# Performance work log

Measured on AMD Instinct MI355X. Metric: run time of the kernel, lower is better.

The kernel has to match this reference:

```python
import jax, jax.numpy as jnp
import numpy as np

N, T, H = 4000, 32, 64      # N = batch_size*n_neurons, t_repetition, gcn_d
E = 1024000
NT = N * T                   # graph nodes after temporal unrolling
N_NEURONS = 500
B = N // N_NEURONS
T_EBD = 16                   # tau * t_repetition = 0.5*32
N_STEPS = 12


def setup_inputs() -> dict:
    key = jax.random.key(0)
    ks = jax.random.split(key, 13)
    s = 1.0 / np.sqrt(H)
    return {
        "node_features": jax.random.normal(ks[0], (N, T, H), jnp.float32),
        "edge_index_batch": jax.random.randint(ks[1], (2, E), 0, NT, jnp.int32),
        "edge_attr_batch": jax.random.uniform(ks[2], (E,), jnp.float32),
        "batch": jax.random.randint(ks[3], (N,), 0, B, jnp.int32),
        # GRU params (1 layer, torch layout: W_ih [3H,H], W_hh [3H,H])
        "gru_Wih": jax.random.normal(ks[4], (3 * H, H), jnp.float32) * s,
        "gru_Whh": jax.random.normal(ks[5], (3 * H, H), jnp.float32) * s,
        "gru_bih": jax.random.normal(ks[6], (3 * H,), jnp.float32) * s,
        "gru_bhh": jax.random.normal(ks[7], (3 * H,), jnp.float32) * s,
        # GCNConv linear weight [out,in], no bias
        "gcn_W": jax.random.normal(ks[8], (H, H), jnp.float32) * s,
        # temporal attention MLP: Linear(T->T_ebd), Linear(T_ebd->T), no bias
        "attn_W1": jax.random.normal(ks[9], (T_EBD, T), jnp.float32) * (1.0 / np.sqrt(T)),
        "attn_W2": jax.random.normal(ks[10], (T, T_EBD), jnp.float32) * (1.0 / np.sqrt(T_EBD)),
        # final head Linear(gcn_d -> n_steps) with bias
        "fc_W": jax.random.normal(ks[11], (N_STEPS, H), jnp.float32) * s,
        "fc_b": jax.random.normal(ks[12], (N_STEPS,), jnp.float32) * s,
    }


def _gru(x, Wih, Whh, bih, bhh):
    # x: [N, T, H] -> outputs [N, T, H] (torch GRU equations, h0 = 0)
    xg = x @ Wih.T + bih  # [N, T, 3H], input projection precomputed

    def step(h, xg_t):
        hg = h @ Whh.T + bhh
        xr, xz, xn = jnp.split(xg_t, 3, axis=-1)
        hr, hz, hn = jnp.split(hg, 3, axis=-1)
        r = jax.nn.sigmoid(xr + hr)
        z = jax.nn.sigmoid(xz + hz)
        n = jnp.tanh(xn + r * hn)
        h_new = (1.0 - z) * n + z * h
        return h_new, h_new

    h0 = jnp.zeros((x.shape[0], Whh.shape[1]), x.dtype)
    _, hs = jax.lax.scan(step, h0, jnp.swapaxes(xg, 0, 1))  # hs: [T, N, H]
    return jnp.swapaxes(hs, 0, 1)


def _gcn(x, W, edge_index, edge_weight, n_nodes):
    # PyG GCNConv: add self-loops (weight 1), symmetric deg^-1/2 norm, no bias
    loops = jnp.arange(n_nodes, dtype=edge_index.dtype)
    src = jnp.concatenate([edge_index[0], loops])
    dst = jnp.concatenate([edge_index[1], loops])
    w = jnp.concatenate([edge_weight, jnp.ones((n_nodes,), edge_weight.dtype)])
    xw = x @ W.T                                            # [NT, H]
    deg = jax.ops.segment_sum(w, dst, num_segments=n_nodes)
    dis = jnp.where(deg > 0, jax.lax.rsqrt(jnp.where(deg > 0, deg, 1.0)), 0.0)
    norm = dis[src] * w * dis[dst]                          # [E+NT]
    msgs = norm[:, None] * xw[src]                          # gather + scale
    return jax.ops.segment_sum(msgs, dst, num_segments=n_nodes)


def reference(node_features, edge_index_batch, edge_attr_batch, batch,
              gru_Wih, gru_Whh, gru_bih, gru_bhh, gcn_W,
              attn_W1, attn_W2, fc_W, fc_b):
    # DGRLayer: GRU over time, then GCN over the flattened (node,time) graph
    g = _gru(node_features, gru_Wih, gru_Whh, gru_bih, gru_bhh)  # [N, T, H]
    x = g.reshape(NT, H)
    x = _gcn(x, gcn_W, edge_index_batch, edge_attr_batch, NT)
    x3 = x.reshape(N, T, H)

    # TemporalAttention (reshape mirrors torch contiguous .view semantics)
    xt = x3.reshape(B, T, N_NEURONS * H).mean(axis=-1)           # [B, T]
    attn = jax.nn.sigmoid(jax.nn.relu(xt @ attn_W1.T) @ attn_W2.T)  # [B, T]

    nf = x3.reshape(B, T, N_NEURONS, H)
    pooled = jnp.sum(attn[:, :, None, None] * nf, axis=(1, 2))   # [B, H]
    return pooled @ fc_W.T + fc_b                                # [B, n_steps]
```

## Files before the change

### kernel.cpp

```cpp
#include <hip/hip_runtime.h>
#include <hip/hip_fp16.h>

#define NNODES   4000
#define TSTEPS   32
#define HDIM     64
#define ECOUNT   1024000
#define NTOT     128000
#define BATCHB   8
#define NNEUR    500
#define TEBD     16
#define NSTEPS   12

#define CNT_SHIFT 44
#define SUM_MASK  ((1ull << CNT_SHIFT) - 1ull)
#define SLOTS     32
#define REC_BLOCKS (NNODES / 16)

typedef _Float16 half8_t __attribute__((ext_vector_type(8)));
typedef float    f32x4_t __attribute__((ext_vector_type(4)));

__device__ __forceinline__ float sigmoidf_(float x) {
    return 1.0f / (1.0f + __expf(-x));
}
__device__ __forceinline__ float tanhf_(float x) {
    return 1.0f - 2.0f / (1.0f + __expf(2.0f * x));
}

__global__ __launch_bounds__(256) void k_recHist(
    const float* __restrict__ x, const float* __restrict__ Wih,
    const float* __restrict__ Whh, const float* __restrict__ bih,
    const float* __restrict__ bhh, const float* __restrict__ Wg,
    _Float16* __restrict__ xwh,
    const int* __restrict__ ei, const float* __restrict__ ea,
    unsigned long long* __restrict__ dc, int2* __restrict__ se32)
{
    __shared__ __align__(16) _Float16 hbuf[2][16 * 72];

    const int tid = threadIdx.x;

    if (blockIdx.x >= REC_BLOCKS) {
        int e = (blockIdx.x - REC_BLOCKS) * 256 + tid;
        int s = ei[e], d = ei[ECOUNT + e];
        float w = ea[e];
        unsigned long long fx = (unsigned long long)(w * 4294967296.0f + 0.5f);
        unsigned long long old = atomicAdd(&dc[d], (1ull << CNT_SHIFT) | fx);
        int r = (int)(old >> CNT_SHIFT);
        if (r < SLOTS)
            se32[d * SLOTS + r] = make_int2(s, __float_as_int(w));
        return;
    }

    const int lane = tid & 63;
    const int wv   = tid >> 6;
    const int c    = lane & 15;
    const int quad = lane >> 4;
    const int n0   = blockIdx.x * 16;

    auto makeB = [&](const float* W, int row, int k0) -> half8_t {
        const float4* p = (const float4*)(W + (size_t)row * HDIM + k0);
        float4 u = p[0], v = p[1];
        half8_t h;
        h[0] = (_Float16)u.x; h[1] = (_Float16)u.y; h[2] = (_Float16)u.z; h[3] = (_Float16)u.w;
        h[4] = (_Float16)v.x; h[5] = (_Float16)v.y; h[6] = (_Float16)v.z; h[7] = (_Float16)v.w;
        return h;
    };

    half8_t Bxr[2], Bxz[2], Bxn[2], Bhr[2], Bhz[2], Bhn[2], Bw[2];
#pragma unroll
    for (int kt = 0; kt < 2; ++kt) {
        int k0 = kt * 32 + quad * 8;
        Bxr[kt] = makeB(Wih, wv * 16 + c, k0);
        Bxz[kt] = makeB(Wih, 64 + wv * 16 + c, k0);
        Bxn[kt] = makeB(Wih, 128 + wv * 16 + c, k0);
        Bhr[kt] = makeB(Whh, wv * 16 + c, k0);
        Bhz[kt] = makeB(Whh, 64 + wv * 16 + c, k0);
        Bhn[kt] = makeB(Whh, 128 + wv * 16 + c, k0);
        Bw[kt]  = makeB(Wg, wv * 16 + c, k0);
    }

    const int f = wv * 16 + c;
    const float brz_r = bih[f] + bhh[f];
    const float brz_z = bih[64 + f] + bhh[64 + f];
    const float bin_  = bih[128 + f];
    const float bhn_  = bhh[128 + f];

    float hreg[4] = {0.f, 0.f, 0.f, 0.f};
    half8_t ah[2];

    const float* xp = x + (size_t)(n0 + c) * (TSTEPS * HDIM) + quad * 8;

    float4 xq0[4], xq1[4];
    {
        const float* p0 = xp;
        xq0[0] = *(const float4*)(p0);      xq0[1] = *(const float4*)(p0 + 4);
        xq0[2] = *(const float4*)(p0 + 32); xq0[3] = *(const float4*)(p0 + 36);
        const float* p1 = xp + HDIM;
        xq1[0] = *(const float4*)(p1);      xq1[1] = *(const float4*)(p1 + 4);
        xq1[2] = *(const float4*)(p1 + 32); xq1[3] = *(const float4*)(p1 + 36);
    }

    auto step = [&](int t, float4* xq) {
        half8_t ax[2];
#pragma unroll
        for (int kt = 0; kt < 2; ++kt) {
            float4 u = xq[kt * 2], v = xq[kt * 2 + 1];
            half8_t a;
            a[0] = (_Float16)u.x; a[1] = (_Float16)u.y; a[2] = (_Float16)u.z; a[3] = (_Float16)u.w;
            a[4] = (_Float16)v.x; a[5] = (_Float16)v.y; a[6] = (_Float16)v.z; a[7] = (_Float16)v.w;
            ax[kt] = a;
        }
        if (t + 2 < TSTEPS) {
            const float* pt = xp + (size_t)(t + 2) * HDIM;
            xq[0] = *(const float4*)(pt);      xq[1] = *(const float4*)(pt + 4);
            xq[2] = *(const float4*)(pt + 32); xq[3] = *(const float4*)(pt + 36);
        }

        f32x4_t Cr  = (f32x4_t){0.f, 0.f, 0.f, 0.f};
        f32x4_t Cz  = (f32x4_t){0.f, 0.f, 0.f, 0.f};
        f32x4_t Cnx = (f32x4_t){0.f, 0.f, 0.f, 0.f};
        f32x4_t Cnh = (f32x4_t){0.f, 0.f, 0.f, 0.f};

#pragma unroll
        for (int kt = 0; kt < 2; ++kt) {
            Cr  = __builtin_amdgcn_mfma_f32_16x16x32_f16(ax[kt], Bxr[kt], Cr, 0, 0, 0);
            Cz  = __builtin_amdgcn_mfma_f32_16x16x32_f16(ax[kt], Bxz[kt], Cz, 0, 0, 0);
            Cnx = __builtin_amdgcn_mfma_f32_16x16x32_f16(ax[kt], Bxn[kt], Cnx, 0, 0, 0);
        }
        if (t > 0) {
#pragma unroll
            for (int kt = 0; kt < 2; ++kt) {
                Cr  = __builtin_amdgcn_mfma_f32_16x16x32_f16(ah[kt], Bhr[kt], Cr, 0, 0, 0);
                Cz  = __builtin_amdgcn_mfma_f32_16x16x32_f16(ah[kt], Bhz[kt], Cz, 0, 0, 0);
                Cnh = __builtin_amdgcn_mfma_f32_16x16x32_f16(ah[kt], Bhn[kt], Cnh, 0, 0, 0);
            }
        }

        _Float16* hb = hbuf[t & 1];
#pragma unroll
        for (int r = 0; r < 4; ++r) {
            float rr = sigmoidf_(Cr[r] + brz_r);
            float zz = sigmoidf_(Cz[r] + brz_z);
            float nn = tanhf_(Cnx[r] + bin_ + rr * (Cnh[r] + bhn_));
            float hn = (1.0f - zz) * nn + zz * hreg[r];
            hreg[r] = hn;
            hb[(quad * 4 + r) * 72 + f] = (_Float16)hn;
        }

        __syncthreads();

#pragma unroll
        for (int kt = 0; kt < 2; ++kt)
            ah[kt] = *(half8_t*)&hb[c * 72 + kt * 32 + quad * 8];

        f32x4_t Cw = (f32x4_t){0.f, 0.f, 0.f, 0.f};
#pragma unroll
        for (int kt = 0; kt < 2; ++kt)
            Cw = __builtin_amdgcn_mfma_f32_16x16x32_f16(ah[kt], Bw[kt], Cw, 0, 0, 0);

#pragma unroll
        for (int r = 0; r < 4; ++r) {
            int row = (n0 + quad * 4 + r) * TSTEPS + t;
            xwh[(size_t)row * HDIM + f] = (_Float16)Cw[r];
        }
    };

#pragma unroll 1
    for (int tt = 0; tt < TSTEPS; tt += 2) {
        step(tt, xq0);
        step(tt + 1, xq1);
    }
}

__global__ void k_dis(const unsigned long long* __restrict__ dc,
                      float* __restrict__ dis) {
    int i = blockIdx.x * blockDim.x + threadIdx.x;
    if (i < NTOT) {
        float deg = 1.0f + (float)(dc[i] & SUM_MASK) * 0x1p-32f;
        dis[i] = rsqrtf(deg);
    }
}

__global__ __launch_bounds__(256) void k_gather(
    const _Float16* __restrict__ xwh, const unsigned long long* __restrict__ dc,
    const int2* __restrict__ se32, const float* __restrict__ dis,
    _Float16* __restrict__ y)
{
    const int lane = threadIdx.x & 63;
    const int d = blockIdx.x * 4 + (threadIdx.x >> 6);
    const float dd = dis[d];
    int cnt = (int)(dc[d] >> CNT_SHIFT);
    cnt = cnt < SLOTS ? cnt : SLOTS;
    const int2* bkt = se32 + (size_t)d * SLOTS;

    float a0 = dd * (float)xwh[(size_t)d * HDIM + lane];
    float a1 = 0.f, a2 = 0.f, a3 = 0.f;
    int j = 0;
    for (; j + 4 <= cnt; j += 4) {
        int2 e0 = bkt[j], e1 = bkt[j + 1], e2 = bkt[j + 2], e3 = bkt[j + 3];
        float c0 = dis[e0.x] * __int_as_float(e0.y);
        float c1 = dis[e1.x] * __int_as_float(e1.y);
        float c2 = dis[e2.x] * __int_as_float(e2.y);
        float c3 = dis[e3.x] * __int_as_float(e3.y);
        float v0 = (float)xwh[(size_t)e0.x * HDIM + lane];
        float v1 = (float)xwh[(size_t)e1.x * HDIM + lane];
        float v2 = (float)xwh[(size_t)e2.x * HDIM + lane];
        float v3 = (float)xwh[(size_t)e3.x * HDIM + lane];
        a0 = fmaf(c0, v0, a0);
        a1 = fmaf(c1, v1, a1);
        a2 = fmaf(c2, v2, a2);
        a3 = fmaf(c3, v3, a3);
    }
    for (; j < cnt; ++j) {
        int2 e = bkt[j];
        a0 = fmaf(dis[e.x] * __int_as_float(e.y),
                  (float)xwh[(size_t)e.x * HDIM + lane], a0);
    }
    y[(size_t)d * HDIM + lane] = (_Float16)(dd * ((a0 + a1) + (a2 + a3)));
}

__global__ __launch_bounds__(256) void k_S(const _Float16* __restrict__ y,
                                           float* __restrict__ S) {
    const int bt = blockIdx.x;
    const int tid = threadIdx.x;
    const int h = tid & 63, g = tid >> 6;
    const _Float16* base = y + (size_t)bt * (NNEUR * HDIM);
    float acc = 0.f;
    for (int n = g; n < NNEUR; n += 4) acc += (float)base[n * HDIM + h];
    __shared__ float red[256];
    red[tid] = acc;
    __syncthreads();
    if (tid < 64)
        S[bt * 64 + tid] = red[tid] + red[64 + tid] + red[128 + tid] + red[192 + tid];
}

__global__ __launch_bounds__(256) void k_final(
    const float* __restrict__ S, const float* __restrict__ W1,
    const float* __restrict__ W2, const float* __restrict__ fcW,
    const float* __restrict__ fcb, float* __restrict__ out)
{
    __shared__ float xt[256];
    __shared__ float a1[128];
    __shared__ float attn[256];
    __shared__ float pooled[512];
    const int tid = threadIdx.x;

    {
        float s = 0.f;
        const float* p = S + tid * 64;
#pragma unroll
        for (int hh = 0; hh < 64; ++hh) s += p[hh];
        xt[tid] = s * (1.0f / 32000.0f);
    }
    __syncthreads();
    if (tid < 128) {
        int b = tid >> 4, i = tid & 15;
        float s = 0.f;
#pragma unroll
        for (int t = 0; t < 32; ++t) s += xt[b * 32 + t] * W1[i * 32 + t];
        a1[tid] = fmaxf(s, 0.f);
    }
    __syncthreads();
    {
        int b = tid >> 5, t = tid & 31;
        float s = 0.f;
#pragma unroll
        for (int i = 0; i < 16; ++i) s += a1[b * 16 + i] * W2[t * 16 + i];
        attn[tid] = 1.0f / (1.0f + __expf(-s));
    }
    __syncthreads();
    for (int o = tid; o < 512; o += 256) {
        int b = o >> 6, h = o & 63;
        float s = 0.f;
#pragma unroll
        for (int t = 0; t < 32; ++t) s += attn[b * 32 + t] * S[(b * 32 + t) * 64 + h];
        pooled[o] = s;
    }
    __syncthreads();
    if (tid < BATCHB * NSTEPS) {
        int b = tid / NSTEPS, st = tid % NSTEPS;
        float acc = fcb[st];
#pragma unroll
        for (int h = 0; h < 64; ++h) acc += pooled[b * 64 + h] * fcW[st * 64 + h];
        out[b * NSTEPS + st] = acc;
    }
}

extern "C" void kernel_launch(void* const* d_in, const int* in_sizes, int n_in,
                              void* d_out, int out_size, void* d_ws, size_t ws_size,
                              hipStream_t stream) {
    const float* x   = (const float*)d_in[0];
    const int*   ei  = (const int*)  d_in[1];
    const float* ea  = (const float*)d_in[2];
    const float* Wih = (const float*)d_in[4];
    const float* Whh = (const float*)d_in[5];
    const float* bih = (const float*)d_in[6];
    const float* bhh = (const float*)d_in[7];
    const float* Wg  = (const float*)d_in[8];
    const float* W1  = (const float*)d_in[9];
    const float* W2  = (const float*)d_in[10];
    const float* fcW = (const float*)d_in[11];
    const float* fcb = (const float*)d_in[12];
    float* out = (float*)d_out;

    char* p = (char*)d_ws;
    unsigned long long* dc = (unsigned long long*)p; p += sizeof(unsigned long long) * NTOT;
    int2*  se32 = (int2*)p;        p += sizeof(int2) * (size_t)NTOT * SLOTS;
    _Float16* xwh = (_Float16*)p;  p += sizeof(_Float16) * (size_t)NTOT * HDIM;
    _Float16* y   = (_Float16*)p;  p += sizeof(_Float16) * (size_t)NTOT * HDIM;
    float* dis = (float*)p;        p += sizeof(float) * NTOT;
    float* S   = (float*)p;

    hipMemsetAsync(dc, 0, sizeof(unsigned long long) * NTOT, stream);
    k_recHist <<<REC_BLOCKS + ECOUNT / 256, 256, 0, stream>>>(
        x, Wih, Whh, bih, bhh, Wg, xwh, ei, ea, dc, se32);
    k_dis     <<<(NTOT + 255) / 256, 256, 0, stream>>>(dc, dis);
    k_gather  <<<NTOT / 4, 256, 0, stream>>>(xwh, dc, se32, dis, y);
    k_S       <<<256, 256, 0, stream>>>(y, S);
    k_final   <<<1, 256, 0, stream>>>(S, W1, W2, fcW, fcb, out);
}
```

Baseline: 273.3 us.

## Fuse degree normalization and per-batch pooling into the GCN gather kernel

```diff
diff --git a/kernel.cpp b/kernel.cpp
--- a/kernel.cpp
+++ b/kernel.cpp
@@ -171,24 +171,17 @@
     }
 }
 
-__global__ void k_dis(const unsigned long long* __restrict__ dc,
-                      float* __restrict__ dis) {
-    int i = blockIdx.x * blockDim.x + threadIdx.x;
-    if (i < NTOT) {
-        float deg = 1.0f + (float)(dc[i] & SUM_MASK) * 0x1p-32f;
-        dis[i] = rsqrtf(deg);
-    }
-}
-
 __global__ __launch_bounds__(256) void k_gather(
     const _Float16* __restrict__ xwh, const unsigned long long* __restrict__ dc,
-    const int2* __restrict__ se32, const float* __restrict__ dis,
-    _Float16* __restrict__ y)
+    const int2* __restrict__ se32, float* __restrict__ S)
 {
-    const int lane = threadIdx.x & 63;
-    const int d = blockIdx.x * 4 + (threadIdx.x >> 6);
-    const float dd = dis[d];
-    int cnt = (int)(dc[d] >> CNT_SHIFT);
+    const int tid  = threadIdx.x;
+    const int lane = tid & 63;
+    const int d = blockIdx.x * 4 + (tid >> 6);
+
+    const unsigned long long pk = dc[d];
+    const float dd = rsqrtf(1.0f + (float)(pk & SUM_MASK) * 0x1p-32f);
+    int cnt = (int)(pk >> CNT_SHIFT);
     cnt = cnt < SLOTS ? cnt : SLOTS;
     const int2* bkt = se32 + (size_t)d * SLOTS;
 
@@ -197,10 +190,12 @@
     int j = 0;
     for (; j + 4 <= cnt; j += 4) {
         int2 e0 = bkt[j], e1 = bkt[j + 1], e2 = bkt[j + 2], e3 = bkt[j + 3];
-        float c0 = dis[e0.x] * __int_as_float(e0.y);
-        float c1 = dis[e1.x] * __int_as_float(e1.y);
-        float c2 = dis[e2.x] * __int_as_float(e2.y);
-        float c3 = dis[e3.x] * __int_as_float(e3.y);
+        unsigned long long p0 = dc[e0.x], p1 = dc[e1.x];
+        unsigned long long p2 = dc[e2.x], p3 = dc[e3.x];
+        float c0 = rsqrtf(1.0f + (float)(p0 & SUM_MASK) * 0x1p-32f) * __int_as_float(e0.y);
+        float c1 = rsqrtf(1.0f + (float)(p1 & SUM_MASK) * 0x1p-32f) * __int_as_float(e1.y);
+        float c2 = rsqrtf(1.0f + (float)(p2 & SUM_MASK) * 0x1p-32f) * __int_as_float(e2.y);
+        float c3 = rsqrtf(1.0f + (float)(p3 & SUM_MASK) * 0x1p-32f) * __int_as_float(e3.y);
         float v0 = (float)xwh[(size_t)e0.x * HDIM + lane];
         float v1 = (float)xwh[(size_t)e1.x * HDIM + lane];
         float v2 = (float)xwh[(size_t)e2.x * HDIM + lane];
@@ -212,25 +207,18 @@
     }
     for (; j < cnt; ++j) {
         int2 e = bkt[j];
-        a0 = fmaf(dis[e.x] * __int_as_float(e.y),
+        unsigned long long pe = dc[e.x];
+        a0 = fmaf(rsqrtf(1.0f + (float)(pe & SUM_MASK) * 0x1p-32f) * __int_as_float(e.y),
                   (float)xwh[(size_t)e.x * HDIM + lane], a0);
     }
-    y[(size_t)d * HDIM + lane] = (_Float16)(dd * ((a0 + a1) + (a2 + a3)));
-}
-
-__global__ __launch_bounds__(256) void k_S(const _Float16* __restrict__ y,
-                                           float* __restrict__ S) {
-    const int bt = blockIdx.x;
-    const int tid = threadIdx.x;
-    const int h = tid & 63, g = tid >> 6;
-    const _Float16* base = y + (size_t)bt * (NNEUR * HDIM);
-    float acc = 0.f;
-    for (int n = g; n < NNEUR; n += 4) acc += (float)base[n * HDIM + h];
+
     __shared__ float red[256];
-    red[tid] = acc;
-    __syncthreads();
-    if (tid < 64)
-        S[bt * 64 + tid] = red[tid] + red[64 + tid] + red[128 + tid] + red[192 + tid];
+    red[tid] = dd * ((a0 + a1) + (a2 + a3));
+    __syncthreads();
+    if (tid < 64) {
+        float s = red[tid] + red[64 + tid] + red[128 + tid] + red[192 + tid];
+        atomicAdd(&S[((blockIdx.x * 4) / NNEUR) * HDIM + tid], s);
+    }
 }
 
 __global__ __launch_bounds__(256) void k_final(
@@ -304,17 +292,13 @@
 
     char* p = (char*)d_ws;
     unsigned long long* dc = (unsigned long long*)p; p += sizeof(unsigned long long) * NTOT;
+    float* S = (float*)p;          p += sizeof(float) * 256 * HDIM;
     int2*  se32 = (int2*)p;        p += sizeof(int2) * (size_t)NTOT * SLOTS;
     _Float16* xwh = (_Float16*)p;  p += sizeof(_Float16) * (size_t)NTOT * HDIM;
-    _Float16* y   = (_Float16*)p;  p += sizeof(_Float16) * (size_t)NTOT * HDIM;
-    float* dis = (float*)p;        p += sizeof(float) * NTOT;
-    float* S   = (float*)p;
-
-    hipMemsetAsync(dc, 0, sizeof(unsigned long long) * NTOT, stream);
+
+    hipMemsetAsync(dc, 0, sizeof(unsigned long long) * NTOT + sizeof(float) * 256 * HDIM, stream);
     k_recHist <<<REC_BLOCKS + ECOUNT / 256, 256, 0, stream>>>(
         x, Wih, Whh, bih, bhh, Wg, xwh, ei, ea, dc, se32);
-    k_dis     <<<(NTOT + 255) / 256, 256, 0, stream>>>(dc, dis);
-    k_gather  <<<NTOT / 4, 256, 0, stream>>>(xwh, dc, se32, dis, y);
-    k_S       <<<256, 256, 0, stream>>>(y, S);
+    k_gather  <<<NTOT / 4, 256, 0, stream>>>(xwh, dc, se32, S);
     k_final   <<<1, 256, 0, stream>>>(S, W1, W2, fcW, fcb, out);
 }
```

Measured after the change: 271.3 us. About the same (-0.7%).
